# Optimization experiments

Hardware: AMD Instinct MI355X
Metric: run time of the kernel (lower is better)

## Reference

```python
import jax, jax.numpy as jnp
import numpy as np

N, E, D_IN, D_H, D_OUT = 8000, 256000, 128, 128, 64
TEMP = 10.0       # config temperature.value (non-learnable)
WEIGHT = 1.0      # config weight.value (non-learnable)
LN_EPS = 1e-5


def _gcn_conv(x, W, b, src, dst, n):
    # PyG GCNConv: add self loops, sym-normalized aggregation, then bias.
    h = x @ W
    loop = jnp.arange(n)
    s = jnp.concatenate([src, loop])
    d = jnp.concatenate([dst, loop])
    deg = jnp.zeros((n,), h.dtype).at[d].add(1.0)
    dinv = jax.lax.rsqrt(jnp.maximum(deg, 1e-12))
    norm = dinv[s] * dinv[d]                       # [E+N]
    out = jax.ops.segment_sum(h[s] * norm[:, None], d, num_segments=n)
    return out + b


def _entropy_gradient(x, A, temperature, normalize):
    # E_i = 0.5 * sum_j A_ij ||x_i - x_j||^2  (dense adjacency, as in repo)
    sq = jnp.sum(x * x, axis=1)                    # [N]
    Ax = A @ x                                     # [N,d]
    deg = A.sum(axis=1)                            # [N]
    En = 0.5 * (deg * sq + A @ sq - 2.0 * jnp.sum(x * Ax, axis=1))
    if normalize:
        En = En / (jnp.max(En) + 1e-12)
    logits = -En / temperature
    P = jax.nn.softmax(logits)
    logP = jax.nn.log_softmax(logits)
    S = -jnp.sum(P * logP)
    c = P * (logP + S) / temperature               # dS/dE_k
    # dS/dx_i = c_i*(deg_i x_i - (Ax)_i) + (A^T c)_i x_i - (A^T (c*x))_i
    ATc = A.T @ c
    return (c[:, None] * (deg[:, None] * x - Ax)
            + ATc[:, None] * x - A.T @ (c[:, None] * x))


def _layer_norm(x, gamma, beta):
    mu = jnp.mean(x, axis=-1, keepdims=True)
    var = jnp.mean(jnp.square(x - mu), axis=-1, keepdims=True)
    return (x - mu) * jax.lax.rsqrt(var + LN_EPS) * gamma + beta


def setup_inputs() -> dict:
    key = jax.random.key(0)
    ks = jax.random.split(key, 6)
    def w(k, i, o):
        return jax.random.normal(k, (i, o), jnp.float32) / np.sqrt(i).astype(np.float32)
    return {
        "x": jax.random.normal(ks[0], (N, D_IN), jnp.float32),
        "edge_index": jax.random.randint(ks[1], (2, E), 0, N),
        "W1": w(ks[2], D_IN, D_H), "b1": jnp.zeros((D_H,), jnp.float32),
        "W2": w(ks[3], D_H, D_H), "b2": jnp.zeros((D_H,), jnp.float32),
        "W_out": w(ks[4], D_H, D_OUT), "b_out": jnp.zeros((D_OUT,), jnp.float32),
        "ln_gamma": jnp.ones((D_H,), jnp.float32),
        "ln_beta": jnp.zeros((D_H,), jnp.float32),
    }


def reference(x, edge_index, W1, b1, W2, b2, W_out, b_out, ln_gamma, ln_beta):
    n = x.shape[0]
    src, dst = edge_index[0], edge_index[1]
    # dense adjacency (to_dense_adj sums duplicate edges)
    A = jnp.zeros((n, n), x.dtype).at[src, dst].add(1.0)
    for W, b in ((W1, b1), (W2, b2)):
        h = _gcn_conv(x, W, b, src, dst, n)
        eg = jax.lax.stop_gradient(_entropy_gradient(h, A, TEMP, True))
        h = h + WEIGHT * eg
        h = jax.nn.relu(h)
        x = _layer_norm(h, ln_gamma, ln_beta)
    embedding = _gcn_conv(x, W_out, b_out, src, dst, n)
    return embedding
```

## Files before the change

kernel.cpp:

```cpp
#include <hip/hip_runtime.h>
#include <hip/hip_bf16.h>

#define DH 128

static constexpr float TEMP_ = 10.0f;
static constexpr float LN_EPS_ = 1e-5f;

__device__ __forceinline__ unsigned short f2bf(float f) {
  union { float f; unsigned int i; } v; v.f = f;
  unsigned int b = v.i + 0x7FFFu + ((v.i >> 16) & 1u);
  return (unsigned short)(b >> 16);
}
__device__ __forceinline__ void dec2(unsigned int u, float& lo, float& hi) {
  union { unsigned int i; float f; } a, b;
  a.i = u << 16; b.i = u & 0xFFFF0000u;
  lo = a.f; hi = b.f;
}
__device__ __forceinline__ void dec8(uint4 u, float* o) {
  dec2(u.x, o[0], o[1]); dec2(u.y, o[2], o[3]);
  dec2(u.z, o[4], o[5]); dec2(u.w, o[6], o[7]);
}
__device__ __forceinline__ unsigned int pack2(float lo, float hi) {
  return (unsigned int)f2bf(lo) | ((unsigned int)f2bf(hi) << 16);
}

__device__ __forceinline__ float grp_sum16(float v) {
  #pragma unroll
  for (int o = 8; o > 0; o >>= 1) v += __shfl_down(v, o, 16);
  return __shfl(v, 0, 16);
}

__global__ __launch_bounds__(256) void k_gemm1_hist(const float* __restrict__ X,
                                                    const float* __restrict__ W,
                                                    unsigned short* __restrict__ Hb,
                                                    const int* __restrict__ ei, int E,
                                                    int* cnt_d, int* cnt_s, int NT) {
  __shared__ float Ws[64 * DH];
  __shared__ float xs[16 * 128];
  const int t = threadIdx.x;
  if ((int)blockIdx.x < NT) {
    const int row0 = blockIdx.x * 16;
    const float4* xg = (const float4*)(X + row0 * 128);
    float4* xs4 = (float4*)xs;
    xs4[t] = xg[t];
    xs4[t + 256] = xg[t + 256];
    const int c = t & 127, rg = t >> 7;
    float acc[8];
    #pragma unroll
    for (int r = 0; r < 8; ++r) acc[r] = 0.f;
    for (int kt = 0; kt < 2; ++kt) {
      __syncthreads();
      for (int i = t; i < 64 * DH; i += 256) Ws[i] = W[kt * 64 * DH + i];
      __syncthreads();
      for (int k = 0; k < 64; ++k) {
        float wv = Ws[k * DH + c];
        #pragma unroll
        for (int r = 0; r < 8; ++r)
          acc[r] += xs[(rg * 8 + r) * 128 + kt * 64 + k] * wv;
      }
    }
    #pragma unroll
    for (int r = 0; r < 8; ++r)
      Hb[(row0 + rg * 8 + r) * DH + c] = f2bf(acc[r]);
  } else {
    const int nb = gridDim.x - NT;
    for (int e = (blockIdx.x - NT) * 256 + t; e < E; e += nb * 256) {
      atomicAdd(&cnt_s[ei[e]], 1);
      atomicAdd(&cnt_d[ei[E + e]], 1);
    }
  }
}

__global__ __launch_bounds__(256) void k_scan_a(const int* __restrict__ cnt_d,
                                                const int* __restrict__ cnt_s,
                                                int* off_d, int* off_s, int* bsum,
                                                float* dinv, float* dego, int n) {
  __shared__ int ws4[4];
  const int t = threadIdx.x;
  const int dir = blockIdx.x >> 5, blk = blockIdx.x & 31;
  const int* cnt = dir ? cnt_s : cnt_d;
  int* off = dir ? off_s : off_d;
  const int NPB = (n + 31) >> 5;
  const int i = blk * NPB + t;
  const bool valid = (t < NPB) && (i < n);
  int tot = valid ? cnt[i] : 0;
  const int lane = t & 63, w = t >> 6;
  int v = tot;
  #pragma unroll
  for (int o = 1; o < 64; o <<= 1) {
    int u = __shfl_up(v, o, 64);
    if (lane >= o) v += u;
  }
  if (lane == 63) ws4[w] = v;
  __syncthreads();
  int wbase = 0;
  #pragma unroll
  for (int k = 0; k < 4; ++k) wbase += (k < w) ? ws4[k] : 0;
  const int excl = wbase + v - tot;
  if (valid) {
    off[i] = excl;
    if (dir == 0) dinv[i] = rsqrtf((float)tot + 1.0f);
    else          dego[i] = (float)tot;
  }
  if (t == 0) {
    int bt = 0;
    #pragma unroll
    for (int k = 0; k < 4; ++k) bt += ws4[k];
    bsum[dir * 32 + blk] = bt;
  }
}

__global__ __launch_bounds__(256) void k_scan_b(int* cnt_d, int* cnt_s,
                                                int* off_d, int* off_s,
                                                const int* __restrict__ bsum, int n) {
  __shared__ int sb;
  const int t = threadIdx.x;
  const int dir = blockIdx.x >> 5, blk = blockIdx.x & 31;
  int* cnt = dir ? cnt_s : cnt_d;
  int* off = dir ? off_s : off_d;
  if (t == 0) {
    int s = 0;
    for (int k = 0; k < blk; ++k) s += bsum[dir * 32 + k];
    sb = s;
  }
  __syncthreads();
  const int bbase = sb;
  const int NPB = (n + 31) >> 5;
  const int i = blk * NPB + t;
  if (t < NPB && i < n) {
    off[i] = bbase + off[i];
    cnt[i] = 0;
  }
  if (t == 1 && blk == 31) {
    int s = 0;
    for (int k = 0; k < 32; ++k) s += bsum[dir * 32 + k];
    off[n] = s;
  }
}

__global__ void k_fill(const int* __restrict__ ei, int E,
                       const int* __restrict__ off_d, const int* __restrict__ off_s,
                       int* cnt_d, int* cnt_s, int* idx_d, int* idx_s) {
  int e = blockIdx.x * blockDim.x + threadIdx.x;
  if (e < E) {
    int s = ei[e], d = ei[E + e];
    int p = atomicAdd(&cnt_d[d], 1);
    idx_d[off_d[d] + p] = s;
    int q = atomicAdd(&cnt_s[s], 1);
    idx_s[off_s[s] + q] = d;
  }
}

__global__ __launch_bounds__(128) void k_conv_agg(const unsigned short* __restrict__ Hb,
                                                  const float* __restrict__ dinv,
                                                  const float* __restrict__ b,
                                                  const int* __restrict__ off_d,
                                                  const int* __restrict__ idx_d,
                                                  float* __restrict__ G,
                                                  unsigned short* __restrict__ Gb,
                                                  float* __restrict__ sq) {
  const int lane = threadIdx.x & 15;
  const int i = blockIdx.x * 8 + (threadIdx.x >> 4);
  const uint4* Hv = (const uint4*)Hb;
  const float di = dinv[i];
  float acc[8];
  {
    float t8[8]; dec8(Hv[i * 16 + lane], t8);
    #pragma unroll
    for (int k = 0; k < 8; ++k) acc[k] = di * t8[k];
  }
  int o = off_d[i];
  const int oe = off_d[i + 1];
  for (; o + 8 <= oe; o += 8) {
    int s[8]; float dv[8]; uint4 r[8];
    #pragma unroll
    for (int j = 0; j < 8; ++j) s[j] = idx_d[o + j];
    #pragma unroll
    for (int j = 0; j < 8; ++j) { r[j] = Hv[s[j] * 16 + lane]; dv[j] = dinv[s[j]]; }
    #pragma unroll
    for (int j = 0; j < 8; ++j) {
      float t8[8]; dec8(r[j], t8);
      #pragma unroll
      for (int k = 0; k < 8; ++k) acc[k] = fmaf(dv[j], t8[k], acc[k]);
    }
  }
  for (; o < oe; ++o) {
    int s = idx_d[o];
    float dvs = dinv[s];
    float t8[8]; dec8(Hv[s * 16 + lane], t8);
    #pragma unroll
    for (int k = 0; k < 8; ++k) acc[k] = fmaf(dvs, t8[k], acc[k]);
  }
  const float4 b0 = ((const float4*)b)[lane * 2];
  const float4 b1 = ((const float4*)b)[lane * 2 + 1];
  float gi[8];
  gi[0] = fmaf(di, acc[0], b0.x); gi[1] = fmaf(di, acc[1], b0.y);
  gi[2] = fmaf(di, acc[2], b0.z); gi[3] = fmaf(di, acc[3], b0.w);
  gi[4] = fmaf(di, acc[4], b1.x); gi[5] = fmaf(di, acc[5], b1.y);
  gi[6] = fmaf(di, acc[6], b1.z); gi[7] = fmaf(di, acc[7], b1.w);
  ((float4*)G)[i * 32 + lane * 2]     = make_float4(gi[0], gi[1], gi[2], gi[3]);
  ((float4*)G)[i * 32 + lane * 2 + 1] = make_float4(gi[4], gi[5], gi[6], gi[7]);
  uint4 gp;
  gp.x = pack2(gi[0], gi[1]); gp.y = pack2(gi[2], gi[3]);
  gp.z = pack2(gi[4], gi[5]); gp.w = pack2(gi[6], gi[7]);
  ((uint4*)Gb)[i * 16 + lane] = gp;
  float s2 = 0.f;
  #pragma unroll
  for (int k = 0; k < 8; ++k) s2 += gi[k] * gi[k];
  s2 = grp_sum16(s2);
  if (lane == 0) sq[i] = s2;
}

__global__ __launch_bounds__(128) void k_ax_en(const float* __restrict__ G,
                                               const unsigned short* __restrict__ Gb,
                                               const float* __restrict__ sq,
                                               const float* __restrict__ dego,
                                               const int* __restrict__ off_s,
                                               const int* __restrict__ idx_s,
                                               float* __restrict__ Ax,
                                               float* __restrict__ En) {
  const int lane = threadIdx.x & 15;
  const int i = blockIdx.x * 8 + (threadIdx.x >> 4);
  const uint4* Gv = (const uint4*)Gb;
  float axf[8];
  #pragma unroll
  for (int k = 0; k < 8; ++k) axf[k] = 0.f;
  float asq = 0.f;
  int o = off_s[i];
  const int oe = off_s[i + 1];
  for (; o + 8 <= oe; o += 8) {
    int s[8]; float qv[8]; uint4 r[8];
    #pragma unroll
    for (int j = 0; j < 8; ++j) s[j] = idx_s[o + j];
    #pragma unroll
    for (int j = 0; j < 8; ++j) { r[j] = Gv[s[j] * 16 + lane]; qv[j] = sq[s[j]]; }
    #pragma unroll
    for (int j = 0; j < 8; ++j) {
      float t8[8]; dec8(r[j], t8);
      asq += qv[j];
      #pragma unroll
      for (int k = 0; k < 8; ++k) axf[k] += t8[k];
    }
  }
  for (; o < oe; ++o) {
    int s = idx_s[o];
    float t8[8]; dec8(Gv[s * 16 + lane], t8);
    asq += sq[s];
    #pragma unroll
    for (int k = 0; k < 8; ++k) axf[k] += t8[k];
  }
  ((float4*)Ax)[i * 32 + lane * 2]     = make_float4(axf[0], axf[1], axf[2], axf[3]);
  ((float4*)Ax)[i * 32 + lane * 2 + 1] = make_float4(axf[4], axf[5], axf[6], axf[7]);
  const float4 g0 = ((const float4*)G)[i * 32 + lane * 2];
  const float4 g1 = ((const float4*)G)[i * 32 + lane * 2 + 1];
  float dot = g0.x * axf[0] + g0.y * axf[1] + g0.z * axf[2] + g0.w * axf[3]
            + g1.x * axf[4] + g1.y * axf[5] + g1.z * axf[6] + g1.w * axf[7];
  dot = grp_sum16(dot);
  if (lane == 0) En[i] = 0.5f * (dego[i] * sq[i] + asq - 2.f * dot);
}

__device__ __forceinline__ float red1024(float v, bool domax, float* sm) {
  #pragma unroll
  for (int o = 32; o > 0; o >>= 1) {
    float u = __shfl_down(v, o, 64);
    v = domax ? fmaxf(v, u) : v + u;
  }
  if ((threadIdx.x & 63) == 0) sm[threadIdx.x >> 6] = v;
  __syncthreads();
  if (threadIdx.x == 0) {
    float r = sm[0];
    for (int k = 1; k < 16; ++k) r = domax ? fmaxf(r, sm[k]) : r + sm[k];
    sm[0] = r;
  }
  __syncthreads();
  float r = sm[0];
  __syncthreads();
  return r;
}

__global__ __launch_bounds__(1024) void k_softc(const float* __restrict__ En,
                                                float* __restrict__ c, int n) {
  __shared__ float sm[16];
  const int t = threadIdx.x;
  float m = -1e30f;
  for (int i = t; i < n; i += 1024) m = fmaxf(m, En[i]);
  m = red1024(m, true, sm);
  const float invden = -1.0f / ((m + 1e-12f) * TEMP_);
  float se = 0.f, sl = 0.f;
  for (int i = t; i < n; i += 1024) {
    float li = En[i] * invden;
    float e = __expf(li);
    se += e; sl += e * li;
  }
  se = red1024(se, false, sm);
  sl = red1024(sl, false, sm);
  const float logZ = __logf(se);
  const float S = logZ - sl / se;
  const float cmul = (1.0f / se) * (1.0f / TEMP_);
  const float cadd = S - logZ;
  for (int i = t; i < n; i += 1024) {
    float li = En[i] * invden;
    c[i] = __expf(li) * cmul * (li + cadd);
  }
}

template <int DOUT>
__global__ __launch_bounds__(256) void k_combine_gemm(const float* __restrict__ G,
                                                      const unsigned short* __restrict__ Gb,
                                                      const float* __restrict__ Ax,
                                                      const float* __restrict__ cv,
                                                      const float* __restrict__ dego,
                                                      const int* __restrict__ off_d,
                                                      const int* __restrict__ idx_d,
                                                      const float* __restrict__ gamma,
                                                      const float* __restrict__ beta,
                                                      const float* __restrict__ W,
                                                      unsigned short* __restrict__ Hb) {
  __shared__ float Ws[32 * DOUT];
  __shared__ float xs[16 * 128];
  const int t = threadIdx.x;
  const int lane = t & 15;
  const int i = blockIdx.x * 16 + (t >> 4);
  const uint4* Gv = (const uint4*)Gb;
  const float4 g0 = ((const float4*)G)[i * 32 + lane * 2];
  const float4 g1 = ((const float4*)G)[i * 32 + lane * 2 + 1];
  const float gi[8] = { g0.x, g0.y, g0.z, g0.w, g1.x, g1.y, g1.z, g1.w };
  float tf[8];
  #pragma unroll
  for (int k = 0; k < 8; ++k) tf[k] = 0.f;
  float atc = 0.f;
  int o = off_d[i];
  const int oe = off_d[i + 1];
  for (; o + 8 <= oe; o += 8) {
    int s[8]; float cs[8]; uint4 r[8];
    #pragma unroll
    for (int j = 0; j < 8; ++j) s[j] = idx_d[o + j];
    #pragma unroll
    for (int j = 0; j < 8; ++j) { r[j] = Gv[s[j] * 16 + lane]; cs[j] = cv[s[j]]; }
    #pragma unroll
    for (int j = 0; j < 8; ++j) {
      atc += cs[j];
      float t8[8]; dec8(r[j], t8);
      #pragma unroll
      for (int k = 0; k < 8; ++k) tf[k] = fmaf(cs[j], t8[k], tf[k]);
    }
  }
  for (; o < oe; ++o) {
    int s = idx_d[o];
    float cs = cv[s];
    atc += cs;
    float t8[8]; dec8(Gv[s * 16 + lane], t8);
    #pragma unroll
    for (int k = 0; k < 8; ++k) tf[k] = fmaf(cs, t8[k], tf[k]);
  }
  const float ci = cv[i];
  const float dg = dego[i];
  const float4 a0 = ((const float4*)Ax)[i * 32 + lane * 2];
  const float4 a1 = ((const float4*)Ax)[i * 32 + lane * 2 + 1];
  const float axi[8] = { a0.x, a0.y, a0.z, a0.w, a1.x, a1.y, a1.z, a1.w };
  float v[8];
  float ssum = 0.f;
  #pragma unroll
  for (int k = 0; k < 8; ++k) {
    v[k] = fmaxf(gi[k] + ci * (dg * gi[k] - axi[k]) + atc * gi[k] - tf[k], 0.f);
    ssum += v[k];
  }
  float mu = grp_sum16(ssum) * (1.f / 128.f);
  float vsum = 0.f;
  #pragma unroll
  for (int k = 0; k < 8; ++k) {
    v[k] -= mu;
    vsum += v[k] * v[k];
  }
  float var = grp_sum16(vsum) * (1.f / 128.f);
  float rs = rsqrtf(var + LN_EPS_);
  const float4 ga0 = ((const float4*)gamma)[lane * 2];
  const float4 ga1 = ((const float4*)gamma)[lane * 2 + 1];
  const float4 be0 = ((const float4*)beta)[lane * 2];
  const float4 be1 = ((const float4*)beta)[lane * 2 + 1];
  float4 o0, o1;
  o0.x = fmaf(v[0] * rs, ga0.x, be0.x); o0.y = fmaf(v[1] * rs, ga0.y, be0.y);
  o0.z = fmaf(v[2] * rs, ga0.z, be0.z); o0.w = fmaf(v[3] * rs, ga0.w, be0.w);
  o1.x = fmaf(v[4] * rs, ga1.x, be1.x); o1.y = fmaf(v[5] * rs, ga1.y, be1.y);
  o1.z = fmaf(v[6] * rs, ga1.z, be1.z); o1.w = fmaf(v[7] * rs, ga1.w, be1.w);

  float* xrow = xs + (t >> 4) * 128 + lane * 8;
  ((float4*)xrow)[0] = o0;
  ((float4*)xrow)[1] = o1;

  const int row0 = blockIdx.x * 16;
  constexpr int RPT = (16 * DOUT) / 256;
  const int c = t % DOUT;
  const int rg = t / DOUT;
  float acc[RPT];
  #pragma unroll
  for (int r = 0; r < RPT; ++r) acc[r] = 0.f;
  for (int kt = 0; kt < 4; ++kt) {
    if (kt) __syncthreads();
    for (int idx = t; idx < 32 * DOUT; idx += 256) Ws[idx] = W[kt * 32 * DOUT + idx];
    __syncthreads();
    for (int k = 0; k < 32; ++k) {
      float wv = Ws[k * DOUT + c];
      #pragma unroll
      for (int r = 0; r < RPT; ++r)
        acc[r] += xs[(rg * RPT + r) * 128 + kt * 32 + k] * wv;
    }
  }
  #pragma unroll
  for (int r = 0; r < RPT; ++r)
    Hb[(row0 + rg * RPT + r) * DOUT + c] = f2bf(acc[r]);
}

__global__ __launch_bounds__(128) void k_final_agg(const unsigned short* __restrict__ Hb,
                                                   const float* __restrict__ dinv,
                                                   const float* __restrict__ bout,
                                                   const int* __restrict__ off_d,
                                                   const int* __restrict__ idx_d,
                                                   float* __restrict__ out) {
  const int lane = threadIdx.x & 7;
  const int i = blockIdx.x * 16 + (threadIdx.x >> 3);
  const uint4* Hv = (const uint4*)Hb;
  const float di = dinv[i];
  float acc[8];
  {
    float t8[8]; dec8(Hv[i * 8 + lane], t8);
    #pragma unroll
    for (int k = 0; k < 8; ++k) acc[k] = di * t8[k];
  }
  int o = off_d[i];
  const int oe = off_d[i + 1];
  for (; o + 8 <= oe; o += 8) {
    int s[8]; float dv[8]; uint4 r[8];
    #pragma unroll
    for (int j = 0; j < 8; ++j) s[j] = idx_d[o + j];
    #pragma unroll
    for (int j = 0; j < 8; ++j) { r[j] = Hv[s[j] * 8 + lane]; dv[j] = dinv[s[j]]; }
    #pragma unroll
    for (int j = 0; j < 8; ++j) {
      float t8[8]; dec8(r[j], t8);
      #pragma unroll
      for (int k = 0; k < 8; ++k) acc[k] = fmaf(dv[j], t8[k], acc[k]);
    }
  }
  for (; o < oe; ++o) {
    int s = idx_d[o];
    float dvs = dinv[s];
    float t8[8]; dec8(Hv[s * 8 + lane], t8);
    #pragma unroll
    for (int k = 0; k < 8; ++k) acc[k] = fmaf(dvs, t8[k], acc[k]);
  }
  const float4 b0 = ((const float4*)bout)[lane * 2];
  const float4 b1 = ((const float4*)bout)[lane * 2 + 1];
  float4 r0, r1;
  r0.x = fmaf(di, acc[0], b0.x); r0.y = fmaf(di, acc[1], b0.y);
  r0.z = fmaf(di, acc[2], b0.z); r0.w = fmaf(di, acc[3], b0.w);
  r1.x = fmaf(di, acc[4], b1.x); r1.y = fmaf(di, acc[5], b1.y);
  r1.z = fmaf(di, acc[6], b1.z); r1.w = fmaf(di, acc[7], b1.w);
  ((float4*)out)[i * 16 + lane * 2]     = r0;
  ((float4*)out)[i * 16 + lane * 2 + 1] = r1;
}

extern "C" void kernel_launch(void* const* d_in, const int* in_sizes, int n_in,
                              void* d_out, int out_size, void* d_ws, size_t ws_size,
                              hipStream_t stream) {
  const float* x    = (const float*)d_in[0];
  const int*   ei   = (const int*)d_in[1];
  const float* W1   = (const float*)d_in[2];
  const float* b1   = (const float*)d_in[3];
  const float* W2   = (const float*)d_in[4];
  const float* b2   = (const float*)d_in[5];
  const float* Wout = (const float*)d_in[6];
  const float* bout = (const float*)d_in[7];
  const float* gam  = (const float*)d_in[8];
  const float* bet  = (const float*)d_in[9];
  float* out = (float*)d_out;

  const int N = in_sizes[0] / DH;
  const int E = in_sizes[1] / 2;

  float* ws = (float*)d_ws;
  float* G  = ws;   ws += N * DH;
  float* Ax = ws;   ws += N * DH;
  float* sq = ws;   ws += N;
  float* En = ws;   ws += N;
  float* cv = ws;   ws += N;
  float* dinv = ws; ws += N;
  float* dego = ws; ws += N;
  unsigned short* Hb = (unsigned short*)ws; ws += N * DH / 2;
  unsigned short* Gb = (unsigned short*)ws; ws += N * DH / 2;
  int* cnt_d  = (int*)ws; ws += N;
  int* cnt_s  = (int*)ws; ws += N;
  int* off_d  = (int*)ws; ws += N + 4;
  int* off_s  = (int*)ws; ws += N + 4;
  int* bsum   = (int*)ws; ws += 64;
  int* idx_d  = (int*)ws; ws += E;
  int* idx_s  = (int*)ws; ws += E;

  const int NT = N / 16;

  hipMemsetAsync(cnt_d, 0, 2 * N * sizeof(int), stream);
  k_gemm1_hist<<<NT + 256, 256, 0, stream>>>(x, W1, Hb, ei, E, cnt_d, cnt_s, NT);
  k_scan_a<<<64, 256, 0, stream>>>(cnt_d, cnt_s, off_d, off_s, bsum, dinv, dego, N);
  k_scan_b<<<64, 256, 0, stream>>>(cnt_d, cnt_s, off_d, off_s, bsum, N);
  k_fill<<<(E + 255) / 256, 256, 0, stream>>>(ei, E, off_d, off_s, cnt_d, cnt_s,
                                              idx_d, idx_s);

  k_conv_agg<<<N / 8, 128, 0, stream>>>(Hb, dinv, b1, off_d, idx_d, G, Gb, sq);
  k_ax_en<<<N / 8, 128, 0, stream>>>(G, Gb, sq, dego, off_s, idx_s, Ax, En);
  k_softc<<<1, 1024, 0, stream>>>(En, cv, N);
  k_combine_gemm<128><<<N / 16, 256, 0, stream>>>(G, Gb, Ax, cv, dego, off_d,
                                                  idx_d, gam, bet, W2, Hb);
  k_conv_agg<<<N / 8, 128, 0, stream>>>(Hb, dinv, b2, off_d, idx_d, G, Gb, sq);
  k_ax_en<<<N / 8, 128, 0, stream>>>(G, Gb, sq, dego, off_s, idx_s, Ax, En);
  k_softc<<<1, 1024, 0, stream>>>(En, cv, N);
  k_combine_gemm<64><<<N / 16, 256, 0, stream>>>(G, Gb, Ax, cv, dego, off_d,
                                                 idx_d, gam, bet, Wout, Hb);
  k_final_agg<<<N / 16, 128, 0, stream>>>(Hb, dinv, bout, off_d, idx_d, out);
}
```

Baseline: 247.8 us.

## Reorder node processing by degree via counting-sort permutation for load balance

Adds a single-block counting sort per direction that builds a permutation of nodes grouped by in-degree or out-degree. All aggregation kernels then map their thread groups through that permutation, so nodes sharing a wavefront or block have similar edge counts and less divergence in their loops. This costs an extra serial-ish kernel launch on the critical path, an extra indirection per row, and scattered output writes instead of contiguous ones. Because atomics in the sort make the order nondeterministic, rows within a block are also less cache-local.

```diff
diff --git a/kernel.cpp b/kernel.cpp
--- a/kernel.cpp
+++ b/kernel.cpp
@@ -138,6 +138,45 @@
   }
 }
 
+__global__ __launch_bounds__(1024) void k_sort(const int* __restrict__ off_d,
+                                               const int* __restrict__ off_s,
+                                               int* perm_d, int* perm_s, int n) {
+  __shared__ int bins[1024];
+  __shared__ int wsum[16];
+  const int t = threadIdx.x;
+  const int* off = blockIdx.x ? off_s : off_d;
+  int* perm = blockIdx.x ? perm_s : perm_d;
+  bins[t] = 0;
+  __syncthreads();
+  for (int i = t; i < n; i += 1024) {
+    int d = off[i + 1] - off[i];
+    atomicAdd(&bins[d < 1023 ? d : 1023], 1);
+  }
+  __syncthreads();
+  int v = bins[t];
+  const int lane = t & 63, w = t >> 6;
+  int s = v;
+  #pragma unroll
+  for (int o = 1; o < 64; o <<= 1) {
+    int u = __shfl_up(s, o, 64);
+    if (lane >= o) s += u;
+  }
+  if (lane == 63) wsum[w] = s;
+  __syncthreads();
+  int base = 0;
+  for (int k = 0; k < 16; ++k) base += (k < w) ? wsum[k] : 0;
+  int excl = base + s - v;
+  __syncthreads();
+  bins[t] = excl;
+  __syncthreads();
+  for (int i = t; i < n; i += 1024) {
+    int d = off[i + 1] - off[i];
+    d = d < 1023 ? d : 1023;
+    int pos = atomicAdd(&bins[d], 1);
+    perm[pos] = i;
+  }
+}
+
 __global__ void k_fill(const int* __restrict__ ei, int E,
                        const int* __restrict__ off_d, const int* __restrict__ off_s,
                        int* cnt_d, int* cnt_s, int* idx_d, int* idx_s) {
@@ -156,11 +195,12 @@
                                                   const float* __restrict__ b,
                                                   const int* __restrict__ off_d,
                                                   const int* __restrict__ idx_d,
+                                                  const int* __restrict__ perm,
                                                   float* __restrict__ G,
                                                   unsigned short* __restrict__ Gb,
                                                   float* __restrict__ sq) {
   const int lane = threadIdx.x & 15;
-  const int i = blockIdx.x * 8 + (threadIdx.x >> 4);
+  const int i = perm[blockIdx.x * 8 + (threadIdx.x >> 4)];
   const uint4* Hv = (const uint4*)Hb;
   const float di = dinv[i];
   float acc[8];
@@ -217,10 +257,11 @@
                                                const float* __restrict__ dego,
                                                const int* __restrict__ off_s,
                                                const int* __restrict__ idx_s,
+                                               const int* __restrict__ perm,
                                                float* __restrict__ Ax,
                                                float* __restrict__ En) {
   const int lane = threadIdx.x & 15;
-  const int i = blockIdx.x * 8 + (threadIdx.x >> 4);
+  const int i = perm[blockIdx.x * 8 + (threadIdx.x >> 4)];
   const uint4* Gv = (const uint4*)Gb;
   float axf[8];
   #pragma unroll
@@ -312,15 +353,19 @@
                                                       const float* __restrict__ dego,
                                                       const int* __restrict__ off_d,
                                                       const int* __restrict__ idx_d,
+                                                      const int* __restrict__ perm,
                                                       const float* __restrict__ gamma,
                                                       const float* __restrict__ beta,
                                                       const float* __restrict__ W,
                                                       unsigned short* __restrict__ Hb) {
   __shared__ float Ws[32 * DOUT];
   __shared__ float xs[16 * 128];
+  __shared__ int nid[16];
   const int t = threadIdx.x;
+  if (t < 16) nid[t] = perm[blockIdx.x * 16 + t];
+  __syncthreads();
   const int lane = t & 15;
-  const int i = blockIdx.x * 16 + (t >> 4);
+  const int i = nid[t >> 4];
   const uint4* Gv = (const uint4*)Gb;
   const float4 g0 = ((const float4*)G)[i * 32 + lane * 2];
   const float4 g1 = ((const float4*)G)[i * 32 + lane * 2 + 1];
@@ -388,7 +433,6 @@
   ((float4*)xrow)[0] = o0;
   ((float4*)xrow)[1] = o1;
 
-  const int row0 = blockIdx.x * 16;
   constexpr int RPT = (16 * DOUT) / 256;
   const int c = t % DOUT;
   const int rg = t / DOUT;
@@ -408,7 +452,7 @@
   }
   #pragma unroll
   for (int r = 0; r < RPT; ++r)
-    Hb[(row0 + rg * RPT + r) * DOUT + c] = f2bf(acc[r]);
+    Hb[nid[rg * RPT + r] * DOUT + c] = f2bf(acc[r]);
 }
 
 __global__ __launch_bounds__(128) void k_final_agg(const unsigned short* __restrict__ Hb,
@@ -416,9 +460,10 @@
                                                    const float* __restrict__ bout,
                                                    const int* __restrict__ off_d,
                                                    const int* __restrict__ idx_d,
+                                                   const int* __restrict__ perm,
                                                    float* __restrict__ out) {
   const int lane = threadIdx.x & 7;
-  const int i = blockIdx.x * 16 + (threadIdx.x >> 3);
+  const int i = perm[blockIdx.x * 16 + (threadIdx.x >> 3)];
   const uint4* Hv = (const uint4*)Hb;
   const float di = dinv[i];
   float acc[8];
@@ -492,6 +537,8 @@
   int* cnt_s  = (int*)ws; ws += N;
   int* off_d  = (int*)ws; ws += N + 4;
   int* off_s  = (int*)ws; ws += N + 4;
+  int* perm_d = (int*)ws; ws += N;
+  int* perm_s = (int*)ws; ws += N;
   int* bsum   = (int*)ws; ws += 64;
   int* idx_d  = (int*)ws; ws += E;
   int* idx_s  = (int*)ws; ws += E;
@@ -502,18 +549,23 @@
   k_gemm1_hist<<<NT + 256, 256, 0, stream>>>(x, W1, Hb, ei, E, cnt_d, cnt_s, NT);
   k_scan_a<<<64, 256, 0, stream>>>(cnt_d, cnt_s, off_d, off_s, bsum, dinv, dego, N);
   k_scan_b<<<64, 256, 0, stream>>>(cnt_d, cnt_s, off_d, off_s, bsum, N);
+  k_sort<<<2, 1024, 0, stream>>>(off_d, off_s, perm_d, perm_s, N);
   k_fill<<<(E + 255) / 256, 256, 0, stream>>>(ei, E, off_d, off_s, cnt_d, cnt_s,
                                               idx_d, idx_s);
 
-  k_conv_agg<<<N / 8, 128, 0, stream>>>(Hb, dinv, b1, off_d, idx_d, G, Gb, sq);
-  k_ax_en<<<N / 8, 128, 0, stream>>>(G, Gb, sq, dego, off_s, idx_s, Ax, En);
+  k_conv_agg<<<N / 8, 128, 0, stream>>>(Hb, dinv, b1, off_d, idx_d, perm_d,
+                                        G, Gb, sq);
+  k_ax_en<<<N / 8, 128, 0, stream>>>(G, Gb, sq, dego, off_s, idx_s, perm_s,
+                                     Ax, En);
   k_softc<<<1, 1024, 0, stream>>>(En, cv, N);
   k_combine_gemm<128><<<N / 16, 256, 0, stream>>>(G, Gb, Ax, cv, dego, off_d,
-                                                  idx_d, gam, bet, W2, Hb);
-  k_conv_agg<<<N / 8, 128, 0, stream>>>(Hb, dinv, b2, off_d, idx_d, G, Gb, sq);
-  k_ax_en<<<N / 8, 128, 0, stream>>>(G, Gb, sq, dego, off_s, idx_s, Ax, En);
+                                                  idx_d, perm_d, gam, bet, W2, Hb);
+  k_conv_agg<<<N / 8, 128, 0, stream>>>(Hb, dinv, b2, off_d, idx_d, perm_d,
+                                        G, Gb, sq);
+  k_ax_en<<<N / 8, 128, 0, stream>>>(G, Gb, sq, dego, off_s, idx_s, perm_s,
+                                     Ax, En);
   k_softc<<<1, 1024, 0, stream>>>(En, cv, N);
   k_combine_gemm<64><<<N / 16, 256, 0, stream>>>(G, Gb, Ax, cv, dego, off_d,
-                                                 idx_d, gam, bet, Wout, Hb);
-  k_final_agg<<<N / 16, 128, 0, stream>>>(Hb, dinv, bout, off_d, idx_d, out);
-}
+                                                 idx_d, perm_d, gam, bet, Wout, Hb);
+  k_final_agg<<<N / 16, 128, 0, stream>>>(Hb, dinv, bout, off_d, idx_d, perm_d, out);
+}
```

Result: slower. 254.6 us (+2.7%).
